# Optimization experiments

Measured on AMD Instinct MI355X. Metric: run time of the kernel, lower is better.

The kernel has to match this reference:

```python
import jax, jax.numpy as jnp
import numpy as np

B, N, C, H = 2, 2048, 1024, 16
D = C // H  # head dim = 64
EPS = 1e-12  # torch F.normalize eps


def l2norm(t):
    # F.normalize(t, dim=-1): x / max(||x||_2, eps)
    n = jnp.linalg.norm(t, axis=-1, keepdims=True)
    return t / jnp.maximum(n, EPS)


def setup_inputs() -> dict:
    key = jax.random.key(0)
    k1, k2, k3 = jax.random.split(key, 3)
    x = jax.random.normal(k1, (B, N, C), dtype=jnp.float32)
    qkv_w = jax.random.normal(k2, (3 * C, C), dtype=jnp.float32) * (1.0 / np.sqrt(C))
    temperature = jnp.ones((H, 1, 1), dtype=jnp.float32)
    proj_w = jax.random.normal(k3, (C, C), dtype=jnp.float32) * (1.0 / np.sqrt(C))
    proj_b = jnp.zeros((C,), dtype=jnp.float32)
    return {"x": x, "qkv_w": qkv_w, "temperature": temperature,
            "proj_w": proj_w, "proj_b": proj_b}


def reference(x, qkv_w, temperature, proj_w, proj_b):
    b, n, c = x.shape
    qkv = jnp.einsum('bnc,fc->bnf', x, qkv_w)           # [B,N,3C], no bias
    q, k, v = jnp.split(qkv, 3, axis=-1)                # each [B,N,C]
    # l2-normalize over FULL channel dim (before head split), as in source
    q = l2norm(q)
    k = l2norm(k)
    # split heads -> [B,H,N,D]
    q = q.reshape(b, n, H, D).transpose(0, 2, 1, 3)
    k = k.reshape(b, n, H, D).transpose(0, 2, 1, 3)
    v = v.reshape(b, n, H, D).transpose(0, 2, 1, 3)
    scale = 1.0 / np.sqrt(D)
    q = q * scale
    k = k * scale
    attn = jnp.einsum('bhnd,bhkd->bhnk', q, k)          # [B,H,N,N]
    attn = attn / temperature                           # (H,1,1) broadcasts
    attn = jax.nn.softmax(attn, axis=-1)
    out = jnp.einsum('bhnk,bhkd->bhnd', attn, v)        # [B,H,N,D]
    out = out.transpose(0, 2, 1, 3).reshape(b, n, c)    # [B,N,C]
    out = jnp.einsum('bnc,oc->bno', out, proj_w) + proj_b
    return out
```

## Files before the change

### kernel.cpp

```cpp
#include <hip/hip_runtime.h>

typedef __bf16 bf16;
using bf16x2 = __attribute__((ext_vector_type(2))) bf16;
using bf16x4 = __attribute__((ext_vector_type(4))) bf16;
using bf16x8 = __attribute__((ext_vector_type(8))) bf16;
using f32x4  = __attribute__((ext_vector_type(4))) float;

#define DEVI __device__ __forceinline__

DEVI void gload_lds16(const void* g, void* l) {
  __builtin_amdgcn_global_load_lds((const __attribute__((address_space(1))) void*)g,
                                   (__attribute__((address_space(3))) void*)l, 16, 0, 0);
}

DEVI float exp2_fast(float x) { return __builtin_amdgcn_exp2f(x); }

__global__ __launch_bounds__(256) void k_cvt(const float* __restrict__ in,
                                             bf16* __restrict__ out) {
  int i = blockIdx.x * 256 + threadIdx.x;
  f32x4 v = ((const f32x4*)in)[i];
  bf16x4 o = {(bf16)v.x, (bf16)v.y, (bf16)v.z, (bf16)v.w};
  ((bf16x4*)out)[i] = o;
}

template<int OUT_BF16, int HAS_BIAS>
__global__ __launch_bounds__(256) void k_gemm_bt(
    const bf16* __restrict__ A, const bf16* __restrict__ W,
    const float* __restrict__ bias, void* __restrict__ outp,
    int Kk, int Nout)
{
  __shared__ __align__(16) bf16 As[128 * 32];
  __shared__ __align__(16) bf16 Bs[128 * 32];
  const int t = threadIdx.x;
  const int lane = t & 63, wv = t >> 6;
  const int l15 = lane & 15, l4 = lane >> 4;
  const int row0 = blockIdx.x * 128, col0 = blockIdx.y * 128;
  const int wr = wv >> 1, wc = wv & 1;

  f32x4 acc[4][4];
  #pragma unroll
  for (int m = 0; m < 4; ++m)
    #pragma unroll
    for (int n = 0; n < 4; ++n) acc[m][n] = (f32x4){0.f, 0.f, 0.f, 0.f};

  const int g0 = t, g1 = t + 256;
  const bf16* ga0 = A + (size_t)(row0 + (g0 >> 2)) * Kk + (g0 & 3) * 8;
  const bf16* ga1 = A + (size_t)(row0 + (g1 >> 2)) * Kk + (g1 & 3) * 8;
  const bf16* gb0 = W + (size_t)(col0 + (g0 >> 2)) * Kk + (g0 & 3) * 8;
  const bf16* gb1 = W + (size_t)(col0 + (g1 >> 2)) * Kk + (g1 & 3) * 8;
  char* la0 = (char*)As + wv * 1024;
  char* la1 = (char*)As + 4096 + wv * 1024;
  char* lb0 = (char*)Bs + wv * 1024;
  char* lb1 = (char*)Bs + 4096 + wv * 1024;

  const int nk = Kk >> 5;
  for (int kt = 0; kt < nk; ++kt) {
    __syncthreads();
    gload_lds16(ga0 + kt * 32, la0);
    gload_lds16(ga1 + kt * 32, la1);
    gload_lds16(gb0 + kt * 32, lb0);
    gload_lds16(gb1 + kt * 32, lb1);
    __syncthreads();
    bf16x8 af[4], bfv[4];
    #pragma unroll
    for (int m = 0; m < 4; ++m)
      af[m] = *(const bf16x8*)(As + (wr * 64 + m * 16 + l15) * 32 + l4 * 8);
    #pragma unroll
    for (int n = 0; n < 4; ++n)
      bfv[n] = *(const bf16x8*)(Bs + (wc * 64 + n * 16 + l15) * 32 + l4 * 8);
    #pragma unroll
    for (int m = 0; m < 4; ++m)
      #pragma unroll
      for (int n = 0; n < 4; ++n)
        acc[m][n] = __builtin_amdgcn_mfma_f32_16x16x32_bf16(af[m], bfv[n], acc[m][n], 0, 0, 0);
  }

  #pragma unroll
  for (int n = 0; n < 4; ++n) {
    const int col = col0 + wc * 64 + n * 16 + l15;
    float bv = HAS_BIAS ? bias[col] : 0.f;
    #pragma unroll
    for (int m = 0; m < 4; ++m) {
      #pragma unroll
      for (int r = 0; r < 4; ++r) {
        const int row = row0 + wr * 64 + m * 16 + l4 * 4 + r;
        float v = acc[m][n][r] + bv;
        if (OUT_BF16) ((bf16*)outp)[(size_t)row * Nout + col] = (bf16)v;
        else          ((float*)outp)[(size_t)row * Nout + col] = v;
      }
    }
  }
}

__global__ __launch_bounds__(256) void k_rownorm(const bf16* __restrict__ qkv,
                                                 float* __restrict__ invq,
                                                 float* __restrict__ invk)
{
  const int row = blockIdx.x * 4 + (threadIdx.x >> 6);
  const int lane = threadIdx.x & 63;
  const bf16* p = qkv + (size_t)row * 3072 + lane * 16;
  float sq = 0.f, sk = 0.f;
  bf16x8 a0 = *(const bf16x8*)(p);
  bf16x8 a1 = *(const bf16x8*)(p + 8);
  bf16x8 b0 = *(const bf16x8*)(p + 1024);
  bf16x8 b1 = *(const bf16x8*)(p + 1032);
  #pragma unroll
  for (int j = 0; j < 8; ++j) {
    float x0 = (float)a0[j], x1 = (float)a1[j];
    float y0 = (float)b0[j], y1 = (float)b1[j];
    sq += x0 * x0 + x1 * x1;
    sk += y0 * y0 + y1 * y1;
  }
  #pragma unroll
  for (int m = 1; m <= 32; m <<= 1) {
    sq += __shfl_xor(sq, m);
    sk += __shfl_xor(sk, m);
  }
  if (lane == 0) {
    invq[row] = 0.125f / fmaxf(sqrtf(sq), 1e-12f);
    invk[row] = 0.125f / fmaxf(sqrtf(sk), 1e-12f);
  }
}

__global__ __launch_bounds__(256) void k_scatter(
    const bf16* __restrict__ qkv, const float* __restrict__ invq,
    const float* __restrict__ invk, const float* __restrict__ temperature,
    bf16* __restrict__ Qh, bf16* __restrict__ Kh, bf16* __restrict__ Vt)
{
  __shared__ __align__(16) bf16 vt[64][72];
  const int t = threadIdx.x;
  const int b = blockIdx.z, h = blockIdx.y;
  const int n0 = blockIdx.x * 64;
  const float tfac = 1.4426950408889634f / temperature[h];
  {
    const int nl = t >> 2;
    const int d0 = (t & 3) << 4;
    const size_t row = (size_t)b * 2048 + n0 + nl;
    const bf16* src = qkv + row * 3072 + h * 64 + d0;
    const float fq = invq[row];
    const float fk = invk[row] * tfac;
    bf16x8 q0 = *(const bf16x8*)(src);
    bf16x8 q1 = *(const bf16x8*)(src + 8);
    bf16x8 k0 = *(const bf16x8*)(src + 1024);
    bf16x8 k1 = *(const bf16x8*)(src + 1032);
    bf16x8 v0 = *(const bf16x8*)(src + 2048);
    bf16x8 v1 = *(const bf16x8*)(src + 2056);
    bf16x8 qo, ko;
    #pragma unroll
    for (int j = 0; j < 8; ++j) {
      qo[j] = (bf16)((float)q0[j] * fq);
      ko[j] = (bf16)((float)k0[j] * fk);
    }
    size_t orow = ((size_t)(b * 16 + h) * 2048 + n0 + nl) * 64 + d0;
    *(bf16x8*)(Qh + orow) = qo;
    *(bf16x8*)(Kh + orow) = ko;
    #pragma unroll
    for (int j = 0; j < 8; ++j) {
      qo[j] = (bf16)((float)q1[j] * fq);
      ko[j] = (bf16)((float)k1[j] * fk);
    }
    *(bf16x8*)(Qh + orow + 8) = qo;
    *(bf16x8*)(Kh + orow + 8) = ko;
    *(bf16x8*)&vt[nl][d0] = v0;
    *(bf16x8*)&vt[nl][d0 + 8] = v1;
  }
  __syncthreads();
  {
    const int d = t >> 2;
    const int nc = (t & 3) << 4;
    bf16x8 o0, o1;
    #pragma unroll
    for (int j = 0; j < 8; ++j) { o0[j] = vt[nc + j][d]; o1[j] = vt[nc + 8 + j][d]; }
    size_t obase = ((size_t)(b * 16 + h) * 64 + d) * 2048 + n0 + nc;
    *(bf16x8*)(Vt + obase) = o0;
    *(bf16x8*)(Vt + obase + 8) = o1;
  }
}

__global__ __launch_bounds__(512, 4) void k_attn(
    const bf16* __restrict__ Qh, const bf16* __restrict__ Kh,
    const bf16* __restrict__ Vt, bf16* __restrict__ ao)
{
  __shared__ __align__(16) bf16 Kb[2][64 * 64];
  __shared__ __align__(16) bf16 Vb[2][64 * 64];
  __shared__ __align__(16) bf16 Pl[8][16 * 64];
  const int t = threadIdx.x, lane = t & 63, wv = t >> 6;
  const int l15 = lane & 15, l4 = lane >> 4;

  const int bid = blockIdx.x;
  const int swz = (bid & 7) * 64 + (bid >> 3);
  const int plane_id = swz >> 4;
  const int qb = swz & 15;
  const int b = plane_id >> 4, h = plane_id & 15;
  const int q0 = qb * 128 + wv * 16;

  const size_t plane = (size_t)plane_id * (2048 * 64);
  const bf16* Qp = Qh + plane;
  const bf16* Kp = Kh + plane;
  const bf16* Vp = Vt + plane;

  const int srow = t >> 3;
  const int sc = (t & 7) ^ (srow & 7);
  const bf16* gK = Kp + (size_t)srow * 64 + sc * 8;
  const bf16* gV = Vp + (size_t)srow * 2048 + sc * 8;
  char* lK0 = (char*)&Kb[0][0] + wv * 1024;
  char* lK1 = (char*)&Kb[1][0] + wv * 1024;
  char* lV0 = (char*)&Vb[0][0] + wv * 1024;
  char* lV1 = (char*)&Vb[1][0] + wv * 1024;

  bf16x8 qf0 = *(const bf16x8*)(Qp + (q0 + l15) * 64 + l4 * 8);
  bf16x8 qf1 = *(const bf16x8*)(Qp + (q0 + l15) * 64 + 32 + l4 * 8);

  bf16x8 vones;
  #pragma unroll
  for (int j = 0; j < 8; ++j) vones[j] = (bf16)1.0f;

  f32x4 accO[4];
  #pragma unroll
  for (int df = 0; df < 4; ++df) accO[df] = (f32x4){0.f, 0.f, 0.f, 0.f};
  f32x4 accS = (f32x4){0.f, 0.f, 0.f, 0.f};

  bf16* pw = &Pl[wv][0] + l15 * 64;
  const int pxor = (l15 & 7) << 3;

#define STAGE(bi, kv0_)                                           \
  do {                                                            \
    gload_lds16(gK + (size_t)(kv0_) * 64, (bi) ? lK1 : lK0);      \
    gload_lds16(gV + (kv0_),              (bi) ? lV1 : lV0);      \
  } while (0)

  STAGE(0, 0);
  __syncthreads();

  int cur = 0;
  for (int kt = 0; kt < 32; ++kt) {
    if (kt < 31) STAGE(cur ^ 1, (kt + 1) * 64);

    const bf16* kb = &Kb[cur][0];
    const bf16* vb = &Vb[cur][0];

    f32x4 s[4];
    #pragma unroll
    for (int kvf = 0; kvf < 4; ++kvf) {
      const int row = kvf * 16 + l15;
      const int r7 = row & 7;
      bf16x8 kf0 = *(const bf16x8*)(kb + row * 64 + ((l4 ^ r7) * 8));
      bf16x8 kf1 = *(const bf16x8*)(kb + row * 64 + (((4 + l4) ^ r7) * 8));
      s[kvf] = (f32x4){0.f, 0.f, 0.f, 0.f};
      s[kvf] = __builtin_amdgcn_mfma_f32_16x16x32_bf16(kf0, qf0, s[kvf], 0, 0, 0);
      s[kvf] = __builtin_amdgcn_mfma_f32_16x16x32_bf16(kf1, qf1, s[kvf], 0, 0, 0);
    }
    #pragma unroll
    for (int kvf = 0; kvf < 4; ++kvf)
      #pragma unroll
      for (int rp = 0; rp < 2; ++rp) {
        bf16x2 pv = {(bf16)exp2_fast(s[kvf][2 * rp]),
                     (bf16)exp2_fast(s[kvf][2 * rp + 1])};
        *(bf16x2*)(pw + ((kvf * 16 + l4 * 4 + 2 * rp) ^ pxor)) = pv;
      }
    #pragma unroll
    for (int ss = 0; ss < 2; ++ss) {
      bf16x8 pf = *(const bf16x8*)(pw + (((ss * 32 + l4 * 8)) ^ pxor));
      accS = __builtin_amdgcn_mfma_f32_16x16x32_bf16(pf, vones, accS, 0, 0, 0);
      #pragma unroll
      for (int df = 0; df < 4; ++df) {
        const int row = df * 16 + l15;
        bf16x8 vf = *(const bf16x8*)(vb + row * 64 + (((ss * 4 + l4) ^ (row & 7)) * 8));
        accO[df] = __builtin_amdgcn_mfma_f32_16x16x32_bf16(pf, vf, accO[df], 0, 0, 0);
      }
    }
    __syncthreads();
    cur ^= 1;
  }
#undef STAGE

  #pragma unroll
  for (int r = 0; r < 4; ++r) {
    const float inv = 1.f / accS[r];
    const size_t orow = ((size_t)b * 2048 + q0 + l4 * 4 + r) * 1024 + h * 64;
    #pragma unroll
    for (int df = 0; df < 4; ++df)
      ao[orow + df * 16 + l15] = (bf16)(accO[df][r] * inv);
  }
}

extern "C" void kernel_launch(void* const* d_in, const int* in_sizes, int n_in,
                              void* d_out, int out_size, void* d_ws, size_t ws_size,
                              hipStream_t stream)
{
  (void)in_sizes; (void)n_in; (void)out_size; (void)ws_size;
  const float* x      = (const float*)d_in[0];
  const float* qkv_w  = (const float*)d_in[1];
  const float* temp   = (const float*)d_in[2];
  const float* proj_w = (const float*)d_in[3];
  const float* proj_b = (const float*)d_in[4];
  float* out = (float*)d_out;

  char* w = (char*)d_ws;
  auto take = [&](size_t bytes) { char* p = w; w += (bytes + 255) & ~(size_t)255; return p; };
  bf16*  xb    = (bf16*)take((size_t)4096 * 1024 * 2);
  bf16*  wqkvb = (bf16*)take((size_t)3072 * 1024 * 2);
  bf16*  wpb   = (bf16*)take((size_t)1024 * 1024 * 2);
  bf16*  qkvb  = (bf16*)take((size_t)4096 * 3072 * 2);
  float* invq  = (float*)take((size_t)4096 * 4);
  float* invk  = (float*)take((size_t)4096 * 4);
  bf16*  Qh    = (bf16*)take((size_t)32 * 2048 * 64 * 2);
  bf16*  Kh    = (bf16*)take((size_t)32 * 2048 * 64 * 2);
  bf16*  Vt    = (bf16*)take((size_t)32 * 64 * 2048 * 2);
  bf16*  ao    = (bf16*)take((size_t)4096 * 1024 * 2);

  k_cvt<<<4096, 256, 0, stream>>>(x, xb);
  k_cvt<<<3072, 256, 0, stream>>>(qkv_w, wqkvb);
  k_cvt<<<1024, 256, 0, stream>>>(proj_w, wpb);
  k_gemm_bt<1, 0><<<dim3(32, 24), 256, 0, stream>>>(xb, wqkvb, nullptr, qkvb, 1024, 3072);
  k_rownorm<<<1024, 256, 0, stream>>>(qkvb, invq, invk);
  k_scatter<<<dim3(32, 16, 2), 256, 0, stream>>>(qkvb, invq, invk, temp, Qh, Kh, Vt);
  k_attn<<<512, 512, 0, stream>>>(Qh, Kh, Vt, ao);
  k_gemm_bt<0, 1><<<dim3(32, 8), 256, 0, stream>>>(ao, wpb, proj_b, out, 1024, 1024);
}
```

Measured before the change: 203.8 us.

## Process two query tiles per wave in attention to reuse K/V fragments

The attention kernel moves from 8 waves of 16 query rows each to 4 waves of 32 query rows each. Every wave now computes two 16-row score tiles and reuses each K and V LDS fragment read for both. Each thread issues twice as many global-to-LDS loads to fill the same K/V tiles. This halves LDS read traffic per MFMA and the number of threads per block, but doubles accumulator registers and lowers the launch-bounds occupancy hint.

After: 208.6 us. 2.4% more time.

```diff
diff --git a/kernel.cpp b/kernel.cpp
--- a/kernel.cpp
+++ b/kernel.cpp
@@ -177,7 +177,7 @@
   }
 }
 
-__global__ __launch_bounds__(512, 4) void k_attn(
+__global__ __launch_bounds__(256, 2) void k_attn(
     const bf16* __restrict__ Qh, const bf16* __restrict__ Kh,
     const bf16* __restrict__ Vt, bf16* __restrict__ ao)
 {
@@ -192,41 +192,49 @@
   const int plane_id = swz >> 4;
   const int qb = swz & 15;
   const int b = plane_id >> 4, h = plane_id & 15;
-  const int q0 = qb * 128 + wv * 16;
+  const int q0 = qb * 128 + wv * 32;
 
   const size_t plane = (size_t)plane_id * (2048 * 64);
   const bf16* Qp = Qh + plane;
   const bf16* Kp = Kh + plane;
   const bf16* Vp = Vt + plane;
 
-  const int srow = t >> 3;
-  const int sc = (t & 7) ^ (srow & 7);
-  const bf16* gK = Kp + (size_t)srow * 64 + sc * 8;
-  const bf16* gV = Vp + (size_t)srow * 2048 + sc * 8;
-  char* lK0 = (char*)&Kb[0][0] + wv * 1024;
-  char* lK1 = (char*)&Kb[1][0] + wv * 1024;
-  char* lV0 = (char*)&Vb[0][0] + wv * 1024;
-  char* lV1 = (char*)&Vb[1][0] + wv * 1024;
-
-  bf16x8 qf0 = *(const bf16x8*)(Qp + (q0 + l15) * 64 + l4 * 8);
-  bf16x8 qf1 = *(const bf16x8*)(Qp + (q0 + l15) * 64 + 32 + l4 * 8);
+  const int c0 = t, c1 = t + 256;
+  const int r0 = c0 >> 3, r1 = c1 >> 3;
+  const int s0 = (c0 & 7) ^ (r0 & 7), s1 = (c1 & 7) ^ (r1 & 7);
+  const bf16* gK0 = Kp + (size_t)r0 * 64 + s0 * 8;
+  const bf16* gK1 = Kp + (size_t)r1 * 64 + s1 * 8;
+  const bf16* gV0 = Vp + (size_t)r0 * 2048 + s0 * 8;
+  const bf16* gV1 = Vp + (size_t)r1 * 2048 + s1 * 8;
+
+  bf16x8 qf00 = *(const bf16x8*)(Qp + (q0 + l15) * 64 + l4 * 8);
+  bf16x8 qf01 = *(const bf16x8*)(Qp + (q0 + l15) * 64 + 32 + l4 * 8);
+  bf16x8 qf10 = *(const bf16x8*)(Qp + (q0 + 16 + l15) * 64 + l4 * 8);
+  bf16x8 qf11 = *(const bf16x8*)(Qp + (q0 + 16 + l15) * 64 + 32 + l4 * 8);
 
   bf16x8 vones;
   #pragma unroll
   for (int j = 0; j < 8; ++j) vones[j] = (bf16)1.0f;
 
-  f32x4 accO[4];
-  #pragma unroll
-  for (int df = 0; df < 4; ++df) accO[df] = (f32x4){0.f, 0.f, 0.f, 0.f};
-  f32x4 accS = (f32x4){0.f, 0.f, 0.f, 0.f};
-
-  bf16* pw = &Pl[wv][0] + l15 * 64;
+  f32x4 accO0[4], accO1[4];
+  #pragma unroll
+  for (int df = 0; df < 4; ++df) {
+    accO0[df] = (f32x4){0.f, 0.f, 0.f, 0.f};
+    accO1[df] = (f32x4){0.f, 0.f, 0.f, 0.f};
+  }
+  f32x4 accS0 = (f32x4){0.f, 0.f, 0.f, 0.f};
+  f32x4 accS1 = (f32x4){0.f, 0.f, 0.f, 0.f};
+
+  bf16* pw0 = &Pl[wv * 2][0] + l15 * 64;
+  bf16* pw1 = &Pl[wv * 2 + 1][0] + l15 * 64;
   const int pxor = (l15 & 7) << 3;
 
-#define STAGE(bi, kv0_)                                           \
-  do {                                                            \
-    gload_lds16(gK + (size_t)(kv0_) * 64, (bi) ? lK1 : lK0);      \
-    gload_lds16(gV + (kv0_),              (bi) ? lV1 : lV0);      \
+#define STAGE(bi, kv0_)                                                      \
+  do {                                                                       \
+    gload_lds16(gK0 + (size_t)(kv0_) * 64, (char*)&Kb[bi][0] + wv * 1024);   \
+    gload_lds16(gK1 + (size_t)(kv0_) * 64, (char*)&Kb[bi][0] + 4096 + wv * 1024); \
+    gload_lds16(gV0 + (kv0_),              (char*)&Vb[bi][0] + wv * 1024);   \
+    gload_lds16(gV1 + (kv0_),              (char*)&Vb[bi][0] + 4096 + wv * 1024); \
   } while (0)
 
   STAGE(0, 0);
@@ -236,37 +244,46 @@
   for (int kt = 0; kt < 32; ++kt) {
     if (kt < 31) STAGE(cur ^ 1, (kt + 1) * 64);
 
-    const bf16* kb = &Kb[cur][0];
-    const bf16* vb = &Vb[cur][0];
-
-    f32x4 s[4];
+    const bf16* kb = cur ? &Kb[1][0] : &Kb[0][0];
+    const bf16* vb = cur ? &Vb[1][0] : &Vb[0][0];
+
+    f32x4 sA[4], sB[4];
     #pragma unroll
     for (int kvf = 0; kvf < 4; ++kvf) {
       const int row = kvf * 16 + l15;
       const int r7 = row & 7;
       bf16x8 kf0 = *(const bf16x8*)(kb + row * 64 + ((l4 ^ r7) * 8));
       bf16x8 kf1 = *(const bf16x8*)(kb + row * 64 + (((4 + l4) ^ r7) * 8));
-      s[kvf] = (f32x4){0.f, 0.f, 0.f, 0.f};
-      s[kvf] = __builtin_amdgcn_mfma_f32_16x16x32_bf16(kf0, qf0, s[kvf], 0, 0, 0);
-      s[kvf] = __builtin_amdgcn_mfma_f32_16x16x32_bf16(kf1, qf1, s[kvf], 0, 0, 0);
+      sA[kvf] = (f32x4){0.f, 0.f, 0.f, 0.f};
+      sA[kvf] = __builtin_amdgcn_mfma_f32_16x16x32_bf16(kf0, qf00, sA[kvf], 0, 0, 0);
+      sA[kvf] = __builtin_amdgcn_mfma_f32_16x16x32_bf16(kf1, qf01, sA[kvf], 0, 0, 0);
+      sB[kvf] = (f32x4){0.f, 0.f, 0.f, 0.f};
+      sB[kvf] = __builtin_amdgcn_mfma_f32_16x16x32_bf16(kf0, qf10, sB[kvf], 0, 0, 0);
+      sB[kvf] = __builtin_amdgcn_mfma_f32_16x16x32_bf16(kf1, qf11, sB[kvf], 0, 0, 0);
     }
     #pragma unroll
     for (int kvf = 0; kvf < 4; ++kvf)
       #pragma unroll
       for (int rp = 0; rp < 2; ++rp) {
-        bf16x2 pv = {(bf16)exp2_fast(s[kvf][2 * rp]),
-                     (bf16)exp2_fast(s[kvf][2 * rp + 1])};
-        *(bf16x2*)(pw + ((kvf * 16 + l4 * 4 + 2 * rp) ^ pxor)) = pv;
+        bf16x2 pva = {(bf16)exp2_fast(sA[kvf][2 * rp]),
+                      (bf16)exp2_fast(sA[kvf][2 * rp + 1])};
+        *(bf16x2*)(pw0 + ((kvf * 16 + l4 * 4 + 2 * rp) ^ pxor)) = pva;
+        bf16x2 pvb = {(bf16)exp2_fast(sB[kvf][2 * rp]),
+                      (bf16)exp2_fast(sB[kvf][2 * rp + 1])};
+        *(bf16x2*)(pw1 + ((kvf * 16 + l4 * 4 + 2 * rp) ^ pxor)) = pvb;
       }
     #pragma unroll
     for (int ss = 0; ss < 2; ++ss) {
-      bf16x8 pf = *(const bf16x8*)(pw + (((ss * 32 + l4 * 8)) ^ pxor));
-      accS = __builtin_amdgcn_mfma_f32_16x16x32_bf16(pf, vones, accS, 0, 0, 0);
+      bf16x8 pf0 = *(const bf16x8*)(pw0 + ((ss * 32 + l4 * 8) ^ pxor));
+      bf16x8 pf1 = *(const bf16x8*)(pw1 + ((ss * 32 + l4 * 8) ^ pxor));
+      accS0 = __builtin_amdgcn_mfma_f32_16x16x32_bf16(pf0, vones, accS0, 0, 0, 0);
+      accS1 = __builtin_amdgcn_mfma_f32_16x16x32_bf16(pf1, vones, accS1, 0, 0, 0);
       #pragma unroll
       for (int df = 0; df < 4; ++df) {
         const int row = df * 16 + l15;
         bf16x8 vf = *(const bf16x8*)(vb + row * 64 + (((ss * 4 + l4) ^ (row & 7)) * 8));
-        accO[df] = __builtin_amdgcn_mfma_f32_16x16x32_bf16(pf, vf, accO[df], 0, 0, 0);
+        accO0[df] = __builtin_amdgcn_mfma_f32_16x16x32_bf16(pf0, vf, accO0[df], 0, 0, 0);
+        accO1[df] = __builtin_amdgcn_mfma_f32_16x16x32_bf16(pf1, vf, accO1[df], 0, 0, 0);
       }
     }
     __syncthreads();
@@ -276,11 +293,15 @@
 
   #pragma unroll
   for (int r = 0; r < 4; ++r) {
-    const float inv = 1.f / accS[r];
-    const size_t orow = ((size_t)b * 2048 + q0 + l4 * 4 + r) * 1024 + h * 64;
-    #pragma unroll
-    for (int df = 0; df < 4; ++df)
-      ao[orow + df * 16 + l15] = (bf16)(accO[df][r] * inv);
+    const float inv0 = 1.f / accS0[r];
+    const float inv1 = 1.f / accS1[r];
+    const size_t orow0 = ((size_t)b * 2048 + q0 + l4 * 4 + r) * 1024 + h * 64;
+    const size_t orow1 = ((size_t)b * 2048 + q0 + 16 + l4 * 4 + r) * 1024 + h * 64;
+    #pragma unroll
+    for (int df = 0; df < 4; ++df) {
+      ao[orow0 + df * 16 + l15] = (bf16)(accO0[df][r] * inv0);
+      ao[orow1 + df * 16 + l15] = (bf16)(accO1[df][r] * inv1);
+    }
   }
 }
 
@@ -315,6 +336,6 @@
   k_gemm_bt<1, 0><<<dim3(32, 24), 256, 0, stream>>>(xb, wqkvb, nullptr, qkvb, 1024, 3072);
   k_rownorm<<<1024, 256, 0, stream>>>(qkvb, invq, invk);
   k_scatter<<<dim3(32, 16, 2), 256, 0, stream>>>(qkvb, invq, invk, temp, Qh, Kh, Vt);
-  k_attn<<<512, 512, 0, stream>>>(Qh, Kh, Vt, ao);
+  k_attn<<<512, 256, 0, stream>>>(Qh, Kh, Vt, ao);
   k_gemm_bt<0, 1><<<dim3(32, 8), 256, 0, stream>>>(ao, wpb, proj_b, out, 1024, 1024);
 }
```
